# Performance work log

Hardware: AMD Instinct MI355X
Metric: run time of the kernel (lower is better)

The kernel has to match this reference:

```python
import jax, jax.numpy as jnp
import numpy as np

EPS = 1e-5

def _branch(x, W, gamma, beta):
    # 1x1 conv (no bias) + InstanceNorm2d(affine) + ReLU
    y = jnp.einsum('oc,bchw->bohw', W, x)
    mu = y.mean(axis=(2, 3), keepdims=True)
    var = y.var(axis=(2, 3), keepdims=True)
    y = (y - mu) * jax.lax.rsqrt(var + EPS)
    y = y * gamma[None, :, None, None] + beta[None, :, None, None]
    return jax.nn.relu(y)

def setup_inputs() -> dict:
    key = jax.random.key(0)
    ks = jax.random.split(key, 12)
    b, in_ch, h, w = 2, 256, 64, 64
    c = in_ch // 8
    d = dict(
        x1=jax.random.normal(ks[0], (b, in_ch, h, w), jnp.float32),
        x2=jax.random.normal(ks[1], (b, in_ch, h, w), jnp.float32),
        x3=jax.random.normal(ks[2], (b, in_ch, h, w), jnp.float32),
        W1=jax.random.normal(ks[3], (c, in_ch), jnp.float32) * (1.0 / np.sqrt(in_ch)),
        g1=jnp.ones((c,), jnp.float32), b1=jnp.zeros((c,), jnp.float32),
        W2=jax.random.normal(ks[4], (c, in_ch), jnp.float32) * (1.0 / np.sqrt(in_ch)),
        g2=jnp.ones((c,), jnp.float32), b2=jnp.zeros((c,), jnp.float32),
        W3=jax.random.normal(ks[5], (c, in_ch), jnp.float32) * (1.0 / np.sqrt(in_ch)),
        g3=jnp.ones((c,), jnp.float32), b3=jnp.zeros((c,), jnp.float32),
    )
    return d

def _forward(x1, x2, x3, W1, g1, b1, W2, g2, b2, W3, g3, b3):
    q1 = _branch(x1, W1, g1, b1); q2 = _branch(x2, W1, g1, b1); q3 = _branch(x3, W1, g1, b1)
    k1 = _branch(x1, W2, g2, b2); k2 = _branch(x2, W2, g2, b2); k3 = _branch(x3, W2, g2, b2)
    v1 = _branch(x1, W3, g3, b3); v2 = _branch(x2, W3, g3, b3); v3 = _branch(x3, W3, g3, b3)
    b_, c, h, w = q1.shape
    hw = h * w
    Q1 = q1.reshape(b_, c, hw).transpose(0, 2, 1)  # [b,hw,c]
    Q2 = q2.reshape(b_, c, hw).transpose(0, 2, 1)
    Q3 = q3.reshape(b_, c, hw).transpose(0, 2, 1)
    K1 = k1.reshape(b_, c, hw)                      # [b,c,hw]
    K2 = k2.reshape(b_, c, hw)
    K3 = k3.reshape(b_, c, hw)
    sm = lambda Q, K: jax.nn.softmax(jnp.einsum('bic,bcj->bij', Q, K), axis=-1)
    A12 = sm(Q1, K2); A21 = sm(Q2, K1); A23 = sm(Q2, K3)
    A32 = sm(Q3, K2); A13 = sm(Q1, K3)
    # ones[b,c,hw] @ A == broadcast of column-sums of A: track a [b,hw] vector
    colsum = lambda A: A.sum(axis=1)                        # [b,hw]
    step = lambda v, A: jnp.einsum('bk,bkj->bj', v, A)      # [b,hw]
    def bc(v):  # broadcast [b,hw] -> [b,c,h,w]
        return jnp.broadcast_to(v[:, None, :], (b_, c, hw)).reshape(b_, c, h, w)
    p1a = bc(step(step(step(colsum(A12), A23), A32), A21))
    p1b = bc(step(colsum(A12), A21))
    p2 = bc(step(colsum(A23), A32))
    p3a = bc(step(colsum(A12), A23))
    p3b = bc(colsum(A13))
    return (p1a, p1b, p2, p3a, p3b, v1, v2, v3)

def reference(x1, x2, x3, W1, g1, b1, W2, g2, b2, W3, g3, b3):
    return _forward(x1, x2, x3, W1, g1, b1, W2, g2, b2, W3, g3, b3)
```

## Files before the change

### kernel.cpp

```cpp
#include <hip/hip_runtime.h>

typedef unsigned short u16;
typedef u16  u16x8  __attribute__((ext_vector_type(8)));
typedef _Float16 f16x4 __attribute__((ext_vector_type(4)));
typedef _Float16 f16x8 __attribute__((ext_vector_type(8)));
typedef float f32x4 __attribute__((ext_vector_type(4)));

#define HW 4096
#define CIN 256
#define HW32 (HW * 32)
#define L2E 1.4426950408889634f

__device__ __forceinline__ float fexp2(float x) { return __builtin_amdgcn_exp2f(x); }

__global__ __launch_bounds__(256) void convert_kernel(const float* x1, const float* x2, const float* x3,
        const float* W1, const float* W2, const float* W3,
        _Float16* xh, _Float16* wh, float* mean) {
    int bx = blockIdx.x; int t = threadIdx.x;
    if (bx < 1536) {
        int xi = bx >> 9, b = (bx >> 8) & 1, c = bx & 255;
        const float* src = (xi == 0 ? x1 : xi == 1 ? x2 : x3) + (size_t)(b * CIN + c) * HW;
        _Float16* dst = xh + ((size_t)((xi * 2 + b) * CIN) + c) * HW;
        float s = 0.f;
        for (int i = t; i < 1024; i += 256) {
            f32x4 v = ((const f32x4*)src)[i];
            s += v[0] + v[1] + v[2] + v[3];
            f16x4 h;
#pragma unroll
            for (int r = 0; r < 4; ++r) h[r] = (_Float16)v[r];
            ((f16x4*)dst)[i] = h;
        }
        __shared__ float red[256];
        red[t] = s; __syncthreads();
        for (int k = 128; k; k >>= 1) { if (t < k) red[t] += red[t + k]; __syncthreads(); }
        if (t == 0) mean[(xi * 2 + b) * CIN + c] = red[0] * (1.f / HW);
    } else {
        int j = bx - 1536;
        int widx = j >> 1, half = j & 1;
        const float* wsrc = (widx == 0 ? W1 : widx == 1 ? W2 : W3) + half * 4096;
        _Float16* wdst = wh + widx * 8192 + half * 4096;
        for (int i = t; i < 1024; i += 256) {
            f32x4 v = ((const f32x4*)wsrc)[i];
            f16x4 h;
#pragma unroll
            for (int r = 0; r < 4; ++r) h[r] = (_Float16)v[r];
            ((f16x4*)wdst)[i] = h;
        }
    }
}

__global__ __launch_bounds__(256) void m2_kernel(const _Float16* xh, float* Pm2) {
    int xi = blockIdx.y, b = blockIdx.z;
    int xb = xi * 2 + b;
    const _Float16* X = xh + (size_t)xb * CIN * HW;
    int bx = blockIdx.x;
    int chunk = bx >> 4, blk = bx & 15;
    int t = threadIdx.x; int wv = t >> 6; int L = t & 63; int m = L & 15; int quad = L >> 4;
    int region = blk * 4 + wv;
    int r1 = (region >> 3) * 32, r2 = (region & 7) * 32;
    int p0 = chunk * 512 + quad * 8;
    const f16x8* A0 = (const f16x8*)(X + (size_t)(r1 + m) * HW + p0);
    const f16x8* A1 = (const f16x8*)(X + (size_t)(r1 + 16 + m) * HW + p0);
    const f16x8* B0 = (const f16x8*)(X + (size_t)(r2 + m) * HW + p0);
    const f16x8* B1 = (const f16x8*)(X + (size_t)(r2 + 16 + m) * HW + p0);
    f32x4 zero = {0, 0, 0, 0};
    f32x4 acc00 = zero, acc01 = zero, acc10 = zero, acc11 = zero;
#pragma unroll 4
    for (int it = 0; it < 16; ++it) {
        f16x8 a0 = A0[it * 4], a1 = A1[it * 4];
        f16x8 b0 = B0[it * 4], b1 = B1[it * 4];
        acc00 = __builtin_amdgcn_mfma_f32_16x16x32_f16(a0, b0, acc00, 0, 0, 0);
        acc01 = __builtin_amdgcn_mfma_f32_16x16x32_f16(a0, b1, acc01, 0, 0, 0);
        acc10 = __builtin_amdgcn_mfma_f32_16x16x32_f16(a1, b0, acc10, 0, 0, 0);
        acc11 = __builtin_amdgcn_mfma_f32_16x16x32_f16(a1, b1, acc11, 0, 0, 0);
    }
    float* dst = Pm2 + ((size_t)chunk * 6 + xb) * 65536;
#pragma unroll
    for (int r = 0; r < 4; ++r) {
        int row0 = (r1 + quad * 4 + r) * 256, row1 = (r1 + 16 + quad * 4 + r) * 256;
        dst[row0 + r2 + m] = acc00[r];
        dst[row0 + r2 + 16 + m] = acc01[r];
        dst[row1 + r2 + m] = acc10[r];
        dst[row1 + r2 + 16 + m] = acc11[r];
    }
}

__global__ __launch_bounds__(256) void m2combine_kernel(const float* Pm2, float* M2) {
    size_t e = (size_t)blockIdx.x * 256 + threadIdx.x;
    float s = 0.f;
#pragma unroll
    for (int c = 0; c < 8; ++c) s += Pm2[(size_t)c * 6 * 65536 + e];
    M2[e] = s * (1.f / HW);
}

__global__ __launch_bounds__(256) void stats_kernel(const float* M2, const float* mean,
        const float* W1, const float* W2, const float* W3,
        const float* g1, const float* g2, const float* g3,
        const float* b1, const float* b2, const float* b3, float2* afine) {
    int o = blockIdx.x; int xi = blockIdx.y; int b = blockIdx.z;
    int widx = o >> 5; int oc = o & 31;
    const float* Wp = (widx == 0 ? W1 : widx == 1 ? W2 : W3) + oc * CIN;
    const float* gp = (widx == 0 ? g1 : widx == 1 ? g2 : g3);
    const float* bp = (widx == 0 ? b1 : widx == 1 ? b2 : b3);
    int t = threadIdx.x;
    __shared__ float sW[256];
    __shared__ float red[256];
    sW[t] = Wp[t];
    __syncthreads();
    const float* m2row = M2 + ((size_t)(xi * 2 + b) * CIN + t) * CIN;
    float tv = 0.f;
    const f32x4* r4 = (const f32x4*)m2row;
#pragma unroll 4
    for (int k = 0; k < 64; ++k) {
        f32x4 mv = r4[k];
        const f32x4 wv = *(const f32x4*)&sW[k * 4];
        tv += mv[0] * wv[0] + mv[1] * wv[1] + mv[2] * wv[2] + mv[3] * wv[3];
    }
    red[t] = tv * sW[t]; __syncthreads();
    for (int k = 128; k; k >>= 1) { if (t < k) red[t] += red[t + k]; __syncthreads(); }
    float E2 = red[0]; __syncthreads();
    red[t] = sW[t] * mean[(xi * 2 + b) * CIN + t]; __syncthreads();
    for (int k = 128; k; k >>= 1) { if (t < k) red[t] += red[t + k]; __syncthreads(); }
    if (t == 0) {
        float mu = red[0];
        float var = E2 - mu * mu;
        float rsig = rsqrtf(var + 1e-5f);
        float scale = gp[oc] * rsig;
        float bias = bp[oc] - mu * scale;
        if (widx == 0) { scale *= L2E; bias *= L2E; }
        afine[(xi * 2 + b) * 96 + o] = make_float2(scale, bias);
    }
}

__global__ __launch_bounds__(256) void conv_kernel(const _Float16* xh, const _Float16* wh,
        const float2* afine, _Float16* qT, _Float16* kT, float* out) {
    int xi = blockIdx.y, b = blockIdx.z;
    const u16* xb = (const u16*)(xh + (size_t)(xi * 2 + b) * CIN * HW);
    int p0 = blockIdx.x * 64;
    __shared__ u16 lds[32 * 65 * 8];
    int t = threadIdx.x;
    {
        int pc = t & 7, cg = t >> 3;
        u16x8 a[8];
#pragma unroll
        for (int r = 0; r < 8; ++r)
            a[r] = *(const u16x8*)(xb + (size_t)(cg * 8 + r) * HW + p0 + pc * 8);
#pragma unroll
        for (int i = 0; i < 8; ++i) {
            u16x8 d;
#pragma unroll
            for (int r = 0; r < 8; ++r) d[r] = a[r][i];
            int p = pc * 8 + i; int fp = p ^ (p >> 3);
            *(u16x8*)&lds[(cg * 65 + fp) * 8] = d;
        }
    }
    __syncthreads();
    int wv = t >> 6, L = t & 63, m = L & 15, quad = L >> 4;
    int pw0 = wv * 16;
    f16x8 af[8];
    {
        int p = pw0 + m; int fp = p ^ (p >> 3);
#pragma unroll
        for (int k = 0; k < 8; ++k)
            af[k] = *(const f16x8*)&lds[((k * 4 + quad) * 65 + fp) * 8];
    }
    int xb2 = xi * 2 + b;
    for (int ot = 0; ot < 6; ++ot) {
        int o0 = ot * 16; int widx = ot >> 1;
        int o_col = o0 + m;
        f32x4 acc = {0, 0, 0, 0};
#pragma unroll
        for (int k = 0; k < 8; ++k) {
            f16x8 bfr = *(const f16x8*)(wh + (size_t)o_col * CIN + k * 32 + quad * 8);
            acc = __builtin_amdgcn_mfma_f32_16x16x32_f16(af[k], bfr, acc, 0, 0, 0);
        }
        float2 afv = afine[xb2 * 96 + o_col];
        f32x4 vals;
#pragma unroll
        for (int r = 0; r < 4; ++r) {
            float v = acc[r] * afv.x + afv.y;
            vals[r] = v > 0.f ? v : 0.f;
        }
        int prow = p0 + pw0 + quad * 4;
        if (widx < 2) {
            _Float16* dst = (widx == 0 ? qT : kT) + (size_t)xb2 * HW32;
            int cc = (o0 & 31) + m;
#pragma unroll
            for (int r = 0; r < 4; ++r)
                dst[(size_t)(prow + r) * 32 + cc] = (_Float16)vals[r];
        } else {
            float* dst = out + (size_t)(5 + xi) * 262144 + (size_t)b * 131072 + (size_t)(o_col - 64) * HW + prow;
            *(f32x4*)dst = vals;
        }
    }
}

__global__ __launch_bounds__(256) void maxnorm_kernel(const _Float16* qT, const _Float16* kT,
                                                      float* maxq, float* maxk) {
    int id = blockIdx.x;
    int which = id >> 1; int b = id & 1;
    const _Float16* base = (which < 3 ? qT + (size_t)(which * 2 + b) * HW32
                                      : kT + (size_t)((which - 3) * 2 + b) * HW32);
    int t = threadIdx.x;
    float mx = 0.f;
    for (int i = t; i < HW; i += 256) {
        const f16x8* r = (const f16x8*)(base + (size_t)i * 32);
        float s = 0.f;
#pragma unroll
        for (int k = 0; k < 4; ++k) {
            f16x8 v = r[k];
#pragma unroll
            for (int j = 0; j < 8; ++j) { float f = (float)v[j]; s += f * f; }
        }
        mx = fmaxf(mx, s);
    }
    __shared__ float red[256];
    red[t] = mx; __syncthreads();
    for (int k = 128; k; k >>= 1) { if (t < k) red[t] = fmaxf(red[t], red[t + k]); __syncthreads(); }
    if (t == 0) {
        float v = sqrtf(red[0]);
        if (which < 3) maxq[which * 2 + b] = v; else maxk[(which - 3) * 2 + b] = v;
    }
}

__global__ __launch_bounds__(256) void zsweep_kernel(const _Float16* qT, const _Float16* kT,
        const float* maxq, const float* maxk, float* Pz) {
    const int qxA[5] = {0, 1, 1, 2, 0};
    const int kxA[5] = {1, 0, 2, 1, 2};
    int mat = blockIdx.y, b = blockIdx.z;
    const _Float16* qb = qT + (size_t)(qxA[mat] * 2 + b) * HW32;
    const _Float16* kb = kT + (size_t)(kxA[mat] * 2 + b) * HW32;
    float Cg = maxq[qxA[mat] * 2 + b] * maxk[kxA[mat] * 2 + b];
    int bx = blockIdx.x;
    int jc = bx & 15, qblk = bx >> 4;
    int t = threadIdx.x; int wv = t >> 6; int L = t & 63; int m = L & 15; int quad = L >> 4;
    int i0 = qblk * 256 + wv * 64;
    f16x8 a[4];
#pragma unroll
    for (int tt = 0; tt < 4; ++tt)
        a[tt] = *(const f16x8*)(qb + (size_t)(i0 + tt * 16 + m) * 32 + quad * 8);
    const f16x8* kp = (const f16x8*)(kb + m * 32 + quad * 8) + (size_t)jc * (16 * 64);
    f32x4 negC = {-Cg, -Cg, -Cg, -Cg};
    f32x4 zero = {0.f, 0.f, 0.f, 0.f};
    f32x4 z[4] = {zero, zero, zero, zero};
#pragma unroll 4
    for (int j = 0; j < 16; ++j) {
        f16x8 bf = kp[j * 64];
#pragma unroll
        for (int tt = 0; tt < 4; ++tt) {
            f32x4 d = __builtin_amdgcn_mfma_f32_16x16x32_f16(a[tt], bf, negC, 0, 0, 0);
            z[tt][0] += fexp2(d[0]); z[tt][1] += fexp2(d[1]);
            z[tt][2] += fexp2(d[2]); z[tt][3] += fexp2(d[3]);
        }
    }
#pragma unroll
    for (int tt = 0; tt < 4; ++tt)
#pragma unroll
        for (int msk = 1; msk <= 8; msk <<= 1) {
            z[tt][0] += __shfl_xor(z[tt][0], msk); z[tt][1] += __shfl_xor(z[tt][1], msk);
            z[tt][2] += __shfl_xor(z[tt][2], msk); z[tt][3] += __shfl_xor(z[tt][3], msk);
        }
    if (m == 0) {
        int mb = mat * 2 + b;
#pragma unroll
        for (int tt = 0; tt < 4; ++tt) {
            int row = i0 + tt * 16 + quad * 4;
#pragma unroll
            for (int r = 0; r < 4; ++r)
                Pz[((size_t)mb * 16 + jc) * HW + row + r] = z[tt][r];
        }
    }
}

__global__ __launch_bounds__(256) void zcombine_kernel(const float* Pz, float* R, float2* Wa) {
    int mb = blockIdx.y;
    int r = blockIdx.x * 256 + threadIdx.x;
    float Z = 0.f;
#pragma unroll
    for (int c = 0; c < 16; ++c) Z += Pz[((size_t)mb * 16 + c) * HW + r];
    float rz = 1.0f / Z;
    size_t idx = (size_t)mb * HW + r;
    R[idx] = rz;
    if (mb < 2 || mb >= 8) Wa[idx] = make_float2(rz, 0.f);
}

struct PCfg {
    const _Float16* qb; const _Float16* kb;
    const float* mq; const float* mk;
    const float2* wt;
    float2* Pp;
    int nit;
};

__global__ __launch_bounds__(256) void pass2p_kernel(PCfg c0, PCfg c1) {
    PCfg c = (blockIdx.y == 0) ? c0 : c1;
    int b = blockIdx.z;
    int bx = blockIdx.x; int jb = bx & 15; int ic = bx >> 4;
    const _Float16* qb = c.qb + (size_t)b * HW32;
    const _Float16* kb = c.kb + (size_t)b * HW32;
    const float2* wt = c.wt + (size_t)b * HW;
    float Cg = c.mq[b] * c.mk[b];
    int t = threadIdx.x; int wv = t >> 6; int L = t & 63; int m = L & 15; int quad = L >> 4;
    int j0 = jb * 256 + wv * 64;
    f16x8 bf[4];
#pragma unroll
    for (int tt = 0; tt < 4; ++tt)
        bf[tt] = *(const f16x8*)(kb + (size_t)(j0 + tt * 16 + m) * 32 + quad * 8);
    f32x4 negC = {-Cg, -Cg, -Cg, -Cg};
    float a1[4] = {0, 0, 0, 0}, a2[4] = {0, 0, 0, 0};
    int ibase = ic * (c.nit * 16);
#pragma unroll 4
    for (int it = 0; it < c.nit; ++it) {
        int i0 = ibase + it * 16;
        f16x8 av = *(const f16x8*)(qb + (size_t)(i0 + m) * 32 + quad * 8);
        const float2* wr = wt + i0 + quad * 4;
        float2 w0 = wr[0], w1 = wr[1], w2 = wr[2], w3 = wr[3];
#pragma unroll
        for (int tt = 0; tt < 4; ++tt) {
            f32x4 d = __builtin_amdgcn_mfma_f32_16x16x32_f16(av, bf[tt], negC, 0, 0, 0);
            float e0 = fexp2(d[0]), e1 = fexp2(d[1]), e2 = fexp2(d[2]), e3 = fexp2(d[3]);
            a1[tt] += e0 * w0.x + e1 * w1.x + e2 * w2.x + e3 * w3.x;
            a2[tt] += e0 * w0.y + e1 * w1.y + e2 * w2.y + e3 * w3.y;
        }
    }
#pragma unroll
    for (int tt = 0; tt < 4; ++tt) {
        a1[tt] += __shfl_xor(a1[tt], 16); a1[tt] += __shfl_xor(a1[tt], 32);
        a2[tt] += __shfl_xor(a2[tt], 16); a2[tt] += __shfl_xor(a2[tt], 32);
    }
    if (quad == 0) {
        float2* dst = c.Pp + ((size_t)ic * 2 + b) * HW;
#pragma unroll
        for (int tt = 0; tt < 4; ++tt)
            dst[j0 + tt * 16 + m] = make_float2(a1[tt], a2[tt]);
    }
}

__global__ __launch_bounds__(256) void prepA_kernel(const float2* PpA, const float* R,
        float* c12, float* c13, float2* Wa2) {
    int b = blockIdx.y; int j = blockIdx.x * 256 + threadIdx.x;
    float s12 = 0.f, s13 = 0.f;
    for (int ic = 0; ic < 16; ++ic) {
        s12 += PpA[((size_t)ic * 2 + b) * HW + j].x;
        s13 += PpA[((size_t)(16 + ic) * 2 + b) * HW + j].x;
    }
    c12[(size_t)b * HW + j] = s12; c13[(size_t)b * HW + j] = s13;
    float rn = R[((size_t)(2 * 2 + b)) * HW + j];
    Wa2[(size_t)b * HW + j] = make_float2(rn, s12 * rn);
}

__global__ __launch_bounds__(256) void prep_kernel(const float2* Pp, const float* Rn,
        const float* aux, float* o1, float* o2, float2* Wn, int IC, int mode) {
    int b = blockIdx.y; int j = blockIdx.x * 256 + threadIdx.x;
    float s1 = 0.f, s2 = 0.f;
    for (int ic = 0; ic < IC; ++ic) {
        float2 p = Pp[((size_t)ic * 2 + b) * HW + j];
        s1 += p.x; s2 += p.y;
    }
    if (o1) o1[(size_t)b * HW + j] = s1;
    if (o2) o2[(size_t)b * HW + j] = s2;
    if (Wn) {
        float rn = Rn[(size_t)b * HW + j];
        float2 w = (mode == 0) ? make_float2(s1 * rn, s2 * rn)
                               : make_float2(s2 * rn, aux[(size_t)b * HW + j] * rn);
        Wn[(size_t)b * HW + j] = w;
    }
}

__global__ __launch_bounds__(256) void bcast_kernel(const float* vecs, float* out) {
    int bx = blockIdx.x;
    int s = bx >> 6; int rem = bx & 63; int b = rem >> 5; int c = rem & 31;
    const float* src = vecs + ((size_t)s * 2 + b) * HW;
    float* dst = out + ((size_t)(s * 2 + b) * 32 + c) * HW;
    int t = threadIdx.x;
#pragma unroll
    for (int k = 0; k < 4; ++k)
        ((f32x4*)dst)[k * 256 + t] = ((const f32x4*)src)[k * 256 + t];
}

extern "C" void kernel_launch(void* const* d_in, const int* in_sizes, int n_in,
                              void* d_out, int out_size, void* d_ws, size_t ws_size,
                              hipStream_t stream) {
    (void)in_sizes; (void)n_in; (void)out_size; (void)ws_size;
    const float* x1 = (const float*)d_in[0];
    const float* x2 = (const float*)d_in[1];
    const float* x3 = (const float*)d_in[2];
    const float* W1 = (const float*)d_in[3];
    const float* g1 = (const float*)d_in[4];
    const float* b1 = (const float*)d_in[5];
    const float* W2 = (const float*)d_in[6];
    const float* g2 = (const float*)d_in[7];
    const float* b2 = (const float*)d_in[8];
    const float* W3 = (const float*)d_in[9];
    const float* g3 = (const float*)d_in[10];
    const float* b3 = (const float*)d_in[11];
    float* out = (float*)d_out;

    char* w = (char*)d_ws;
    _Float16* xh    = (_Float16*)(w);
    _Float16* wh    = (_Float16*)(w + 12582912);
    float*    mean  = (float*)(w + 12632064);
    float*    M2    = (float*)(w + 12638208);
    float2*   afine = (float2*)(w + 14211072);
    _Float16* qT    = (_Float16*)(w + 14215680);
    _Float16* kT    = (_Float16*)(w + 15788544);
    float*    R     = (float*)(w + 17361408);
    float*    maxq  = (float*)(w + 17525248);
    float*    maxk  = (float*)(w + 17525312);
    float2*   Wa    = (float2*)(w + 17689088);
    float*    vecs  = (float*)(w + 18016768);
    float*    Pz    = (float*)(w + 18213376);
    float2*   PpA   = (float2*)(w + 23456256);
    float2*   PpB   = (float2*)(w + 25553408);
    float2*   PpC   = (float2*)(w + 27650560);
    float2*   PpD   = (float2*)(w + 29747712);
    float*    Pm2   = (float*)(w + 18213376);

    float* v_p1a = vecs + 0 * 2 * HW;
    float* v_p1b = vecs + 1 * 2 * HW;
    float* v_p2  = vecs + 2 * 2 * HW;
    float* v_p3a = vecs + 3 * 2 * HW;
    float* v_p3b = vecs + 4 * 2 * HW;
    float* v_c12 = vecs + 5 * 2 * HW;

    hipLaunchKernelGGL(convert_kernel, dim3(1542), dim3(256), 0, stream,
                       x1, x2, x3, W1, W2, W3, xh, wh, mean);
    hipLaunchKernelGGL(m2_kernel, dim3(128, 3, 2), dim3(256), 0, stream, xh, Pm2);
    hipLaunchKernelGGL(m2combine_kernel, dim3(1536), dim3(256), 0, stream, Pm2, M2);
    hipLaunchKernelGGL(stats_kernel, dim3(96, 3, 2), dim3(256), 0, stream,
                       M2, mean, W1, W2, W3, g1, g2, g3, b1, b2, b3, afine);
    hipLaunchKernelGGL(conv_kernel, dim3(64, 3, 2), dim3(256), 0, stream,
                       xh, wh, afine, qT, kT, out);
    hipLaunchKernelGGL(maxnorm_kernel, dim3(12), dim3(256), 0, stream, qT, kT, maxq, maxk);
    hipLaunchKernelGGL(zsweep_kernel, dim3(256, 5, 2), dim3(256), 0, stream, qT, kT, maxq, maxk, Pz);
    hipLaunchKernelGGL(zcombine_kernel, dim3(16, 10), dim3(256), 0, stream, Pz, R, Wa);

    PCfg cA0 = { qT + 0 * 2 * HW32, kT + 1 * 2 * HW32, maxq + 0, maxk + 2, Wa + 0 * 2 * HW, PpA,               16 };
    PCfg cA1 = { qT + 0 * 2 * HW32, kT + 2 * 2 * HW32, maxq + 0, maxk + 4, Wa + 4 * 2 * HW, PpA + 16 * 2 * HW, 16 };
    hipLaunchKernelGGL(pass2p_kernel, dim3(256, 2, 2), dim3(256), 0, stream, cA0, cA1);
    hipLaunchKernelGGL(prepA_kernel, dim3(16, 2), dim3(256), 0, stream,
                       PpA, R, v_c12, v_p3b, Wa + 2 * 2 * HW);

    PCfg cB = { qT + 1 * 2 * HW32, kT + 2 * 2 * HW32, maxq + 2, maxk + 4, Wa + 2 * 2 * HW, PpB, 8 };
    hipLaunchKernelGGL(pass2p_kernel, dim3(512, 1, 2), dim3(256), 0, stream, cB, cB);
    hipLaunchKernelGGL(prep_kernel, dim3(16, 2), dim3(256), 0, stream,
                       PpB, R + 3 * 2 * HW, (const float*)nullptr,
                       (float*)nullptr, v_p3a, Wa + 3 * 2 * HW, 32, 0);

    PCfg cC = { qT + 2 * 2 * HW32, kT + 1 * 2 * HW32, maxq + 4, maxk + 2, Wa + 3 * 2 * HW, PpC, 8 };
    hipLaunchKernelGGL(pass2p_kernel, dim3(512, 1, 2), dim3(256), 0, stream, cC, cC);
    hipLaunchKernelGGL(prep_kernel, dim3(16, 2), dim3(256), 0, stream,
                       PpC, R + 1 * 2 * HW, v_c12,
                       v_p2, (float*)nullptr, Wa + 1 * 2 * HW, 32, 1);

    PCfg cD = { qT + 1 * 2 * HW32, kT + 0 * 2 * HW32, maxq + 2, maxk + 0, Wa + 1 * 2 * HW, PpD, 8 };
    hipLaunchKernelGGL(pass2p_kernel, dim3(512, 1, 2), dim3(256), 0, stream, cD, cD);
    hipLaunchKernelGGL(prep_kernel, dim3(16, 2), dim3(256), 0, stream,
                       PpD, (const float*)nullptr, (const float*)nullptr,
                       v_p1a, v_p1b, (float2*)nullptr, 32, 0);

    hipLaunchKernelGGL(bcast_kernel, dim3(320), dim3(256), 0, stream, vecs, out);
}
```

Before: 282.2 us.

## Fuse max-norm reduction into conv kernel and specialize pass2 single/dual weight paths

Computes the per-row squared norms of q and k directly in the conv epilogue, reducing them with wave shuffles and a global atomicMax on float bits, so the separate maxnorm kernel and its reread of qT/kT go away. The max buffers are zeroed in convert_kernel, and consumers now take sqrt of the stored squared max. Pass2 gets a flag that skips the second weighted accumulation for the first launch, which only needs one column, and uses packed float2 math elsewhere. This adds atomics and depends on ReLU outputs being non-negative so that integer atomicMax orders the floats correctly.

```diff
diff --git a/kernel.cpp b/kernel.cpp
--- a/kernel.cpp
+++ b/kernel.cpp
@@ -4,6 +4,7 @@
 typedef u16  u16x8  __attribute__((ext_vector_type(8)));
 typedef _Float16 f16x4 __attribute__((ext_vector_type(4)));
 typedef _Float16 f16x8 __attribute__((ext_vector_type(8)));
+typedef float f32x2 __attribute__((ext_vector_type(2)));
 typedef float f32x4 __attribute__((ext_vector_type(4)));
 
 #define HW 4096
@@ -15,7 +16,7 @@
 
 __global__ __launch_bounds__(256) void convert_kernel(const float* x1, const float* x2, const float* x3,
         const float* W1, const float* W2, const float* W3,
-        _Float16* xh, _Float16* wh, float* mean) {
+        _Float16* xh, _Float16* wh, float* mean, float* maxq, float* maxk) {
     int bx = blockIdx.x; int t = threadIdx.x;
     if (bx < 1536) {
         int xi = bx >> 9, b = (bx >> 8) & 1, c = bx & 255;
@@ -36,6 +37,7 @@
         if (t == 0) mean[(xi * 2 + b) * CIN + c] = red[0] * (1.f / HW);
     } else {
         int j = bx - 1536;
+        if (j == 0 && t < 12) { if (t < 6) maxq[t] = 0.f; else maxk[t - 6] = 0.f; }
         int widx = j >> 1, half = j & 1;
         const float* wsrc = (widx == 0 ? W1 : widx == 1 ? W2 : W3) + half * 4096;
         _Float16* wdst = wh + widx * 8192 + half * 4096;
@@ -133,11 +135,13 @@
 }
 
 __global__ __launch_bounds__(256) void conv_kernel(const _Float16* xh, const _Float16* wh,
-        const float2* afine, _Float16* qT, _Float16* kT, float* out) {
+        const float2* afine, _Float16* qT, _Float16* kT, float* out,
+        float* maxq, float* maxk) {
     int xi = blockIdx.y, b = blockIdx.z;
     const u16* xb = (const u16*)(xh + (size_t)(xi * 2 + b) * CIN * HW);
     int p0 = blockIdx.x * 64;
     __shared__ u16 lds[32 * 65 * 8];
+    __shared__ float smq[4], smk[4];
     int t = threadIdx.x;
     {
         int pc = t & 7, cg = t >> 3;
@@ -165,6 +169,7 @@
             af[k] = *(const f16x8*)&lds[((k * 4 + quad) * 65 + fp) * 8];
     }
     int xb2 = xi * 2 + b;
+    float sqq[4] = {0, 0, 0, 0}, sqk[4] = {0, 0, 0, 0};
     for (int ot = 0; ot < 6; ++ot) {
         int o0 = ot * 16; int widx = ot >> 1;
         int o_col = o0 + m;
@@ -188,38 +193,37 @@
 #pragma unroll
             for (int r = 0; r < 4; ++r)
                 dst[(size_t)(prow + r) * 32 + cc] = (_Float16)vals[r];
+            if (widx == 0) {
+#pragma unroll
+                for (int r = 0; r < 4; ++r) sqq[r] += vals[r] * vals[r];
+            } else {
+#pragma unroll
+                for (int r = 0; r < 4; ++r) sqk[r] += vals[r] * vals[r];
+            }
         } else {
             float* dst = out + (size_t)(5 + xi) * 262144 + (size_t)b * 131072 + (size_t)(o_col - 64) * HW + prow;
             *(f32x4*)dst = vals;
         }
     }
-}
-
-__global__ __launch_bounds__(256) void maxnorm_kernel(const _Float16* qT, const _Float16* kT,
-                                                      float* maxq, float* maxk) {
-    int id = blockIdx.x;
-    int which = id >> 1; int b = id & 1;
-    const _Float16* base = (which < 3 ? qT + (size_t)(which * 2 + b) * HW32
-                                      : kT + (size_t)((which - 3) * 2 + b) * HW32);
-    int t = threadIdx.x;
-    float mx = 0.f;
-    for (int i = t; i < HW; i += 256) {
-        const f16x8* r = (const f16x8*)(base + (size_t)i * 32);
-        float s = 0.f;
-#pragma unroll
-        for (int k = 0; k < 4; ++k) {
-            f16x8 v = r[k];
-#pragma unroll
-            for (int j = 0; j < 8; ++j) { float f = (float)v[j]; s += f * f; }
-        }
-        mx = fmaxf(mx, s);
-    }
-    __shared__ float red[256];
-    red[t] = mx; __syncthreads();
-    for (int k = 128; k; k >>= 1) { if (t < k) red[t] = fmaxf(red[t], red[t + k]); __syncthreads(); }
+#pragma unroll
+    for (int msk = 1; msk <= 8; msk <<= 1) {
+#pragma unroll
+        for (int r = 0; r < 4; ++r) {
+            sqq[r] += __shfl_xor(sqq[r], msk);
+            sqk[r] += __shfl_xor(sqk[r], msk);
+        }
+    }
+    float nq = fmaxf(fmaxf(sqq[0], sqq[1]), fmaxf(sqq[2], sqq[3]));
+    float nk = fmaxf(fmaxf(sqk[0], sqk[1]), fmaxf(sqk[2], sqk[3]));
+    nq = fmaxf(nq, __shfl_xor(nq, 16)); nq = fmaxf(nq, __shfl_xor(nq, 32));
+    nk = fmaxf(nk, __shfl_xor(nk, 16)); nk = fmaxf(nk, __shfl_xor(nk, 32));
+    if (L == 0) { smq[wv] = nq; smk[wv] = nk; }
+    __syncthreads();
     if (t == 0) {
-        float v = sqrtf(red[0]);
-        if (which < 3) maxq[which * 2 + b] = v; else maxk[(which - 3) * 2 + b] = v;
+        float bq = fmaxf(fmaxf(smq[0], smq[1]), fmaxf(smq[2], smq[3]));
+        float bk = fmaxf(fmaxf(smk[0], smk[1]), fmaxf(smk[2], smk[3]));
+        atomicMax((unsigned*)&maxq[xb2], __float_as_uint(bq));
+        atomicMax((unsigned*)&maxk[xb2], __float_as_uint(bk));
     }
 }
 
@@ -230,7 +234,7 @@
     int mat = blockIdx.y, b = blockIdx.z;
     const _Float16* qb = qT + (size_t)(qxA[mat] * 2 + b) * HW32;
     const _Float16* kb = kT + (size_t)(kxA[mat] * 2 + b) * HW32;
-    float Cg = maxq[qxA[mat] * 2 + b] * maxk[kxA[mat] * 2 + b];
+    float Cg = sqrtf(maxq[qxA[mat] * 2 + b]) * sqrtf(maxk[kxA[mat] * 2 + b]);
     int bx = blockIdx.x;
     int jc = bx & 15, qblk = bx >> 4;
     int t = threadIdx.x; int wv = t >> 6; int L = t & 63; int m = L & 15; int quad = L >> 4;
@@ -249,8 +253,8 @@
 #pragma unroll
         for (int tt = 0; tt < 4; ++tt) {
             f32x4 d = __builtin_amdgcn_mfma_f32_16x16x32_f16(a[tt], bf, negC, 0, 0, 0);
-            z[tt][0] += fexp2(d[0]); z[tt][1] += fexp2(d[1]);
-            z[tt][2] += fexp2(d[2]); z[tt][3] += fexp2(d[3]);
+            f32x4 e = {fexp2(d[0]), fexp2(d[1]), fexp2(d[2]), fexp2(d[3])};
+            z[tt] = z[tt] + e;
         }
     }
 #pragma unroll
@@ -290,6 +294,7 @@
     const float2* wt;
     float2* Pp;
     int nit;
+    int dual;
 };
 
 __global__ __launch_bounds__(256) void pass2p_kernel(PCfg c0, PCfg c1) {
@@ -298,8 +303,8 @@
     int bx = blockIdx.x; int jb = bx & 15; int ic = bx >> 4;
     const _Float16* qb = c.qb + (size_t)b * HW32;
     const _Float16* kb = c.kb + (size_t)b * HW32;
-    const float2* wt = c.wt + (size_t)b * HW;
-    float Cg = c.mq[b] * c.mk[b];
+    const f32x2* wt = (const f32x2*)(c.wt + (size_t)b * HW);
+    float Cg = sqrtf(c.mq[b]) * sqrtf(c.mk[b]);
     int t = threadIdx.x; int wv = t >> 6; int L = t & 63; int m = L & 15; int quad = L >> 4;
     int j0 = jb * 256 + wv * 64;
     f16x8 bf[4];
@@ -307,32 +312,50 @@
     for (int tt = 0; tt < 4; ++tt)
         bf[tt] = *(const f16x8*)(kb + (size_t)(j0 + tt * 16 + m) * 32 + quad * 8);
     f32x4 negC = {-Cg, -Cg, -Cg, -Cg};
-    float a1[4] = {0, 0, 0, 0}, a2[4] = {0, 0, 0, 0};
+    f32x2 acc[4] = {{0, 0}, {0, 0}, {0, 0}, {0, 0}};
     int ibase = ic * (c.nit * 16);
+    if (c.dual) {
 #pragma unroll 4
-    for (int it = 0; it < c.nit; ++it) {
-        int i0 = ibase + it * 16;
-        f16x8 av = *(const f16x8*)(qb + (size_t)(i0 + m) * 32 + quad * 8);
-        const float2* wr = wt + i0 + quad * 4;
-        float2 w0 = wr[0], w1 = wr[1], w2 = wr[2], w3 = wr[3];
-#pragma unroll
-        for (int tt = 0; tt < 4; ++tt) {
-            f32x4 d = __builtin_amdgcn_mfma_f32_16x16x32_f16(av, bf[tt], negC, 0, 0, 0);
-            float e0 = fexp2(d[0]), e1 = fexp2(d[1]), e2 = fexp2(d[2]), e3 = fexp2(d[3]);
-            a1[tt] += e0 * w0.x + e1 * w1.x + e2 * w2.x + e3 * w3.x;
-            a2[tt] += e0 * w0.y + e1 * w1.y + e2 * w2.y + e3 * w3.y;
+        for (int it = 0; it < c.nit; ++it) {
+            int i0 = ibase + it * 16;
+            f16x8 av = *(const f16x8*)(qb + (size_t)(i0 + m) * 32 + quad * 8);
+            const f32x2* wr = wt + i0 + quad * 4;
+            f32x2 w0 = wr[0], w1 = wr[1], w2 = wr[2], w3 = wr[3];
+#pragma unroll
+            for (int tt = 0; tt < 4; ++tt) {
+                f32x4 d = __builtin_amdgcn_mfma_f32_16x16x32_f16(av, bf[tt], negC, 0, 0, 0);
+                float e0 = fexp2(d[0]), e1 = fexp2(d[1]), e2 = fexp2(d[2]), e3 = fexp2(d[3]);
+                acc[tt] += (f32x2){e0, e0} * w0;
+                acc[tt] += (f32x2){e1, e1} * w1;
+                acc[tt] += (f32x2){e2, e2} * w2;
+                acc[tt] += (f32x2){e3, e3} * w3;
+            }
+        }
+    } else {
+#pragma unroll 4
+        for (int it = 0; it < c.nit; ++it) {
+            int i0 = ibase + it * 16;
+            f16x8 av = *(const f16x8*)(qb + (size_t)(i0 + m) * 32 + quad * 8);
+            const f32x2* wr = wt + i0 + quad * 4;
+            float w0 = wr[0][0], w1 = wr[1][0], w2 = wr[2][0], w3 = wr[3][0];
+#pragma unroll
+            for (int tt = 0; tt < 4; ++tt) {
+                f32x4 d = __builtin_amdgcn_mfma_f32_16x16x32_f16(av, bf[tt], negC, 0, 0, 0);
+                float e0 = fexp2(d[0]), e1 = fexp2(d[1]), e2 = fexp2(d[2]), e3 = fexp2(d[3]);
+                acc[tt][0] += e0 * w0 + e1 * w1 + e2 * w2 + e3 * w3;
+            }
         }
     }
 #pragma unroll
     for (int tt = 0; tt < 4; ++tt) {
-        a1[tt] += __shfl_xor(a1[tt], 16); a1[tt] += __shfl_xor(a1[tt], 32);
-        a2[tt] += __shfl_xor(a2[tt], 16); a2[tt] += __shfl_xor(a2[tt], 32);
+        acc[tt][0] += __shfl_xor(acc[tt][0], 16); acc[tt][0] += __shfl_xor(acc[tt][0], 32);
+        acc[tt][1] += __shfl_xor(acc[tt][1], 16); acc[tt][1] += __shfl_xor(acc[tt][1], 32);
     }
     if (quad == 0) {
         float2* dst = c.Pp + ((size_t)ic * 2 + b) * HW;
 #pragma unroll
         for (int tt = 0; tt < 4; ++tt)
-            dst[j0 + tt * 16 + m] = make_float2(a1[tt], a2[tt]);
+            dst[j0 + tt * 16 + m] = make_float2(acc[tt][0], acc[tt][1]);
     }
 }
 
@@ -424,36 +447,35 @@
     float* v_c12 = vecs + 5 * 2 * HW;
 
     hipLaunchKernelGGL(convert_kernel, dim3(1542), dim3(256), 0, stream,
-                       x1, x2, x3, W1, W2, W3, xh, wh, mean);
+                       x1, x2, x3, W1, W2, W3, xh, wh, mean, maxq, maxk);
     hipLaunchKernelGGL(m2_kernel, dim3(128, 3, 2), dim3(256), 0, stream, xh, Pm2);
     hipLaunchKernelGGL(m2combine_kernel, dim3(1536), dim3(256), 0, stream, Pm2, M2);
     hipLaunchKernelGGL(stats_kernel, dim3(96, 3, 2), dim3(256), 0, stream,
                        M2, mean, W1, W2, W3, g1, g2, g3, b1, b2, b3, afine);
     hipLaunchKernelGGL(conv_kernel, dim3(64, 3, 2), dim3(256), 0, stream,
-                       xh, wh, afine, qT, kT, out);
-    hipLaunchKernelGGL(maxnorm_kernel, dim3(12), dim3(256), 0, stream, qT, kT, maxq, maxk);
+                       xh, wh, afine, qT, kT, out, maxq, maxk);
     hipLaunchKernelGGL(zsweep_kernel, dim3(256, 5, 2), dim3(256), 0, stream, qT, kT, maxq, maxk, Pz);
     hipLaunchKernelGGL(zcombine_kernel, dim3(16, 10), dim3(256), 0, stream, Pz, R, Wa);
 
-    PCfg cA0 = { qT + 0 * 2 * HW32, kT + 1 * 2 * HW32, maxq + 0, maxk + 2, Wa + 0 * 2 * HW, PpA,               16 };
-    PCfg cA1 = { qT + 0 * 2 * HW32, kT + 2 * 2 * HW32, maxq + 0, maxk + 4, Wa + 4 * 2 * HW, PpA + 16 * 2 * HW, 16 };
+    PCfg cA0 = { qT + 0 * 2 * HW32, kT + 1 * 2 * HW32, maxq + 0, maxk + 2, Wa + 0 * 2 * HW, PpA,               16, 0 };
+    PCfg cA1 = { qT + 0 * 2 * HW32, kT + 2 * 2 * HW32, maxq + 0, maxk + 4, Wa + 4 * 2 * HW, PpA + 16 * 2 * HW, 16, 0 };
     hipLaunchKernelGGL(pass2p_kernel, dim3(256, 2, 2), dim3(256), 0, stream, cA0, cA1);
     hipLaunchKernelGGL(prepA_kernel, dim3(16, 2), dim3(256), 0, stream,
                        PpA, R, v_c12, v_p3b, Wa + 2 * 2 * HW);
 
-    PCfg cB = { qT + 1 * 2 * HW32, kT + 2 * 2 * HW32, maxq + 2, maxk + 4, Wa + 2 * 2 * HW, PpB, 8 };
+    PCfg cB = { qT + 1 * 2 * HW32, kT + 2 * 2 * HW32, maxq + 2, maxk + 4, Wa + 2 * 2 * HW, PpB, 8, 1 };
     hipLaunchKernelGGL(pass2p_kernel, dim3(512, 1, 2), dim3(256), 0, stream, cB, cB);
     hipLaunchKernelGGL(prep_kernel, dim3(16, 2), dim3(256), 0, stream,
                        PpB, R + 3 * 2 * HW, (const float*)nullptr,
                        (float*)nullptr, v_p3a, Wa + 3 * 2 * HW, 32, 0);
 
-    PCfg cC = { qT + 2 * 2 * HW32, kT + 1 * 2 * HW32, maxq + 4, maxk + 2, Wa + 3 * 2 * HW, PpC, 8 };
+    PCfg cC = { qT + 2 * 2 * HW32, kT + 1 * 2 * HW32, maxq + 4, maxk + 2, Wa + 3 * 2 * HW, PpC, 8, 1 };
     hipLaunchKernelGGL(pass2p_kernel, dim3(512, 1, 2), dim3(256), 0, stream, cC, cC);
     hipLaunchKernelGGL(prep_kernel, dim3(16, 2), dim3(256), 0, stream,
                        PpC, R + 1 * 2 * HW, v_c12,
                        v_p2, (float*)nullptr, Wa + 1 * 2 * HW, 32, 1);
 
-    PCfg cD = { qT + 1 * 2 * HW32, kT + 0 * 2 * HW32, maxq + 2, maxk + 0, Wa + 1 * 2 * HW, PpD, 8 };
+    PCfg cD = { qT + 1 * 2 * HW32, kT + 0 * 2 * HW32, maxq + 2, maxk + 0, Wa + 1 * 2 * HW, PpD, 8, 1 };
     hipLaunchKernelGGL(pass2p_kernel, dim3(512, 1, 2), dim3(256), 0, stream, cD, cD);
     hipLaunchKernelGGL(prep_kernel, dim3(16, 2), dim3(256), 0, stream,
                        PpD, (const float*)nullptr, (const float*)nullptr,
```

New measurement: 263.2 us. 6.7% less time.
